# Kernel tuning notes

Hardware: AMD Instinct MI355X
Metric: run time of the kernel (lower is better)

## Reference

```python
import jax, jax.numpy as jnp
import numpy as np

N_TIME_INTERVAL = 512
TIME_DIM = 64
PASS_TIME = 1_000_000.0
PER_TIME = PASS_TIME / N_TIME_INTERVAL  # opt-derived bucket width
B, L = 64, 8192


def setup_inputs() -> dict:
    key = jax.random.key(0)
    k1, k2, k3 = jax.random.split(key, 3)
    inp = jax.random.randint(k1, (B, L), 0, 1000, dtype=jnp.int64 if jax.config.jax_enable_x64 else jnp.int32).astype(jnp.int32)
    # gaps uniform in [0, PER_TIME*(N_TIME_INTERVAL-1)) so bucket indices stay in range,
    # timestamps strictly increasing via cumsum (shape [B, L+1])
    gaps = jax.random.uniform(k2, (B, L), dtype=jnp.float32) * (PER_TIME * (N_TIME_INTERVAL - 1))
    t0 = jnp.zeros((B, 1), dtype=jnp.float32)
    timestamp = jnp.concatenate([t0, jnp.cumsum(gaps, axis=1)], axis=1)
    # embedding table == linear_1.weight.T (xavier-normal init), bias zeros
    W = jax.random.normal(k3, (N_TIME_INTERVAL, TIME_DIM), dtype=jnp.float32) * np.sqrt(2.0 / (N_TIME_INTERVAL + TIME_DIM))
    b = jnp.zeros((TIME_DIM,), dtype=jnp.float32)
    return {"input": inp, "timestamp": timestamp, "W": W, "b": b}


def reference(input, timestamp, W, b):
    # pass_time = (t[1:] - t[:-1]) / per_time ; floor ; relu (clamps negatives to 0)
    diff = timestamp[:, 1:] - timestamp[:, :-1]              # [B, L]
    idx = jnp.floor(diff / PER_TIME).astype(jnp.int32)
    idx = jnp.maximum(idx, 0)                                 # relu on int indices
    # scatter one-hot then Linear  ==  gather row of W (= weight.T) plus bias
    time_embedding = W[idx] + b                               # [B, L, TIME_DIM]
    return time_embedding, timestamp[:, :-1]
```

## Files before the change

kernel.cpp:

```cpp
#include <hip/hip_runtime.h>


#define B_DIM 64
#define L_DIM 8192
#define TIME_DIM 64
#define N_TI 512

__global__ __launch_bounds__(256) void IntervalTimeEncoder_77653008712021_kernel(
    const float* __restrict__ ts,
    const float* __restrict__ W,
    const float* __restrict__ bias,
    float* __restrict__ emb,
    float* __restrict__ ts_out)
{
    const int tid = blockIdx.x * blockDim.x + threadIdx.x;
    const int row = tid >> 4;
    const int d4  = tid & 15;
    const int b   = row >> 13;
    const int l   = row & (L_DIM - 1);

    const int ts_base = b * (L_DIM + 1) + l;
    const float t0 = ts[ts_base];
    const float t1 = ts[ts_base + 1];

    const float diff = t1 - t0;
    int idx = (int)floorf(diff / 1953.125f);
    idx = idx < 0 ? 0 : idx;
    idx = idx > (N_TI - 1) ? (N_TI - 1) : idx;

    const float4 w  = reinterpret_cast<const float4*>(W)[idx * (TIME_DIM / 4) + d4];
    const float4 bb = reinterpret_cast<const float4*>(bias)[d4];
    float4 o;
    o.x = w.x + bb.x;
    o.y = w.y + bb.y;
    o.z = w.z + bb.z;
    o.w = w.w + bb.w;
    reinterpret_cast<float4*>(emb)[row * (TIME_DIM / 4) + d4] = o;

    if (d4 == 0) {
        ts_out[row] = t0;
    }
}

extern "C" void kernel_launch(void* const* d_in, const int* in_sizes, int n_in,
                              void* d_out, int out_size, void* d_ws, size_t ws_size,
                              hipStream_t stream) {
    (void)in_sizes; (void)n_in; (void)d_ws; (void)ws_size; (void)out_size;
    const float* ts   = (const float*)d_in[1];
    const float* W    = (const float*)d_in[2];
    const float* bias = (const float*)d_in[3];

    float* emb    = (float*)d_out;
    float* ts_out = (float*)d_out + (size_t)B_DIM * L_DIM * TIME_DIM;

    const int total_threads = B_DIM * L_DIM * (TIME_DIM / 4);
    const int block = 256;
    const int grid  = total_threads / block;

    IntervalTimeEncoder_77653008712021_kernel<<<grid, block, 0, stream>>>(
        ts, W, bias, emb, ts_out);
}
```

Before: 28.92 us.

## Use fixed grid with multi-row per thread, batched loads, nontemporal stores

Replaces the one-thread-per-float4 launch with a fixed 2048x256 grid where each thread handles 16 rows in batches of 4, hoisting the bias load and issuing all timestamp and W loads before the stores. Output stores use nontemporal hints so the 128 MB embedding write does not pollute the cache. This aims to cut per-thread launch and index overhead and raise memory-level parallelism, at the cost of more registers and fewer resident waves.

Measured after the change: 44.58 us. 1.54x slower.

```diff
diff --git a/kernel.cpp b/kernel.cpp
--- a/kernel.cpp
+++ b/kernel.cpp
@@ -6,6 +6,15 @@
 #define TIME_DIM 64
 #define N_TI 512
 
+#define GRID 2048
+#define BLOCK 256
+#define NTHREADS (GRID * BLOCK)
+#define TOTAL_UNITS (B_DIM * L_DIM * (TIME_DIM / 4))
+#define UNITS_PER_THREAD (TOTAL_UNITS / NTHREADS)
+#define ROW_STRIDE (NTHREADS / 16)
+
+typedef float f32x4 __attribute__((ext_vector_type(4)));
+
 __global__ __launch_bounds__(256) void IntervalTimeEncoder_77653008712021_kernel(
     const float* __restrict__ ts,
     const float* __restrict__ W,
@@ -13,32 +22,48 @@
     float* __restrict__ emb,
     float* __restrict__ ts_out)
 {
-    const int tid = blockIdx.x * blockDim.x + threadIdx.x;
-    const int row = tid >> 4;
-    const int d4  = tid & 15;
-    const int b   = row >> 13;
-    const int l   = row & (L_DIM - 1);
+    const int tid  = blockIdx.x * BLOCK + threadIdx.x;
+    const int d4   = tid & 15;
+    const int row0 = tid >> 4;
 
-    const int ts_base = b * (L_DIM + 1) + l;
-    const float t0 = ts[ts_base];
-    const float t1 = ts[ts_base + 1];
+    const f32x4 bb = reinterpret_cast<const f32x4*>(bias)[d4];
+    const f32x4* __restrict__ W4 = reinterpret_cast<const f32x4*>(W);
+    f32x4* __restrict__ emb4 = reinterpret_cast<f32x4*>(emb);
 
-    const float diff = t1 - t0;
-    int idx = (int)floorf(diff / 1953.125f);
-    idx = idx < 0 ? 0 : idx;
-    idx = idx > (N_TI - 1) ? (N_TI - 1) : idx;
+    #pragma unroll
+    for (int k = 0; k < UNITS_PER_THREAD; k += 4) {
+        int   rows[4];
+        float t0[4], t1[4];
 
-    const float4 w  = reinterpret_cast<const float4*>(W)[idx * (TIME_DIM / 4) + d4];
-    const float4 bb = reinterpret_cast<const float4*>(bias)[d4];
-    float4 o;
-    o.x = w.x + bb.x;
-    o.y = w.y + bb.y;
-    o.z = w.z + bb.z;
-    o.w = w.w + bb.w;
-    reinterpret_cast<float4*>(emb)[row * (TIME_DIM / 4) + d4] = o;
+        #pragma unroll
+        for (int j = 0; j < 4; ++j) {
+            const int row  = row0 + (k + j) * ROW_STRIDE;
+            const int b    = row >> 13;
+            const int l    = row & (L_DIM - 1);
+            const int base = b * (L_DIM + 1) + l;
+            rows[j] = row;
+            t0[j] = ts[base];
+            t1[j] = ts[base + 1];
+        }
 
-    if (d4 == 0) {
-        ts_out[row] = t0;
+        f32x4 w[4];
+        #pragma unroll
+        for (int j = 0; j < 4; ++j) {
+            const float diff = t1[j] - t0[j];
+            int idx = (int)floorf(diff / 1953.125f);
+            idx = idx < 0 ? 0 : idx;
+            idx = idx > (N_TI - 1) ? (N_TI - 1) : idx;
+            w[j] = W4[idx * (TIME_DIM / 4) + d4];
+        }
+
+        #pragma unroll
+        for (int j = 0; j < 4; ++j) {
+            f32x4 o = w[j] + bb;
+            __builtin_nontemporal_store(o, &emb4[(size_t)rows[j] * (TIME_DIM / 4) + d4]);
+            if (d4 == 0) {
+                __builtin_nontemporal_store(t0[j], &ts_out[rows[j]]);
+            }
+        }
     }
 }
 
@@ -53,10 +78,6 @@
     float* emb    = (float*)d_out;
     float* ts_out = (float*)d_out + (size_t)B_DIM * L_DIM * TIME_DIM;
 
-    const int total_threads = B_DIM * L_DIM * (TIME_DIM / 4);
-    const int block = 256;
-    const int grid  = total_threads / block;
-
-    IntervalTimeEncoder_77653008712021_kernel<<<grid, block, 0, stream>>>(
+    IntervalTimeEncoder_77653008712021_kernel<<<GRID, BLOCK, 0, stream>>>(
         ts, W, bias, emb, ts_out);
 }
```
